# Performance work log

Hardware: AMD Instinct MI355X
Metric: run time of the kernel (lower is better)

Reference implementation:

```python
import jax, jax.numpy as jnp
import numpy as np
from jax import lax

B, C, L, H = 32, 256, 1280, 5
D = L // H  # head dim = 256
EPS = 1e-5


def setup_inputs() -> dict:
    key = jax.random.key(0)
    ks = jax.random.split(key, 16)
    s = 0.02
    inp = {
        "x": jax.random.normal(ks[0], (B, C, L), jnp.float32),
        # rank encoder Linear(L, L)
        "re_w": jax.random.normal(ks[1], (L, L), jnp.float32) * s,
        "re_b": jnp.zeros((L,), jnp.float32),
        # layer norms
        "ln1_g": jnp.ones((L,), jnp.float32), "ln1_b": jnp.zeros((L,), jnp.float32),
        "ln2_g": jnp.ones((L,), jnp.float32), "ln2_b": jnp.zeros((L,), jnp.float32),
        # attention projections (stored [in, out]; y @ W + b)
        "wq": jax.random.normal(ks[2], (L, L), jnp.float32) * s, "bq": jnp.zeros((L,), jnp.float32),
        "wk": jax.random.normal(ks[3], (L, L), jnp.float32) * s, "bk": jnp.zeros((L,), jnp.float32),
        "wv": jax.random.normal(ks[4], (L, L), jnp.float32) * s, "bv": jnp.zeros((L,), jnp.float32),
        "wo": jax.random.normal(ks[5], (L, L), jnp.float32) * s, "bo": jnp.zeros((L,), jnp.float32),
        # FFN (ffn_size == hidden_size == L in this module)
        "ffn_w1": jax.random.normal(ks[6], (L, L), jnp.float32) * s, "ffn_b1": jnp.zeros((L,), jnp.float32),
        "ffn_w2": jax.random.normal(ks[7], (L, L), jnp.float32) * s, "ffn_b2": jnp.zeros((L,), jnp.float32),
        # Conv1d(C, C, k=3, stride=1, pad=1, bias=False) + BatchNorm1d (eval) + ReLU
        "conv_w": jax.random.normal(ks[8], (C, C, 3), jnp.float32) * (2.0 / (C * 3)) ** 0.5,
        "bn_g": jnp.ones((C,), jnp.float32), "bn_b": jnp.zeros((C,), jnp.float32),
        "bn_m": jnp.zeros((C,), jnp.float32), "bn_v": jnp.ones((C,), jnp.float32),
    }
    return inp


def _layernorm(t, g, b):
    m = jnp.mean(t, axis=-1, keepdims=True)
    v = jnp.var(t, axis=-1, keepdims=True)
    return (t - m) * lax.rsqrt(v + EPS) * g + b


def reference(x, re_w, re_b, ln1_g, ln1_b, ln2_g, ln2_b,
              wq, bq, wk, bk, wv, bv, wo, bo,
              ffn_w1, ffn_b1, ffn_w2, ffn_b2,
              conv_w, bn_g, bn_b, bn_m, bn_v):
    b_, c_, l_ = x.shape
    # _getrank_: rank from double argsort (descending), mapped to (L - rank)/L
    rank_i = jnp.argsort(jnp.argsort(-x, axis=-1), axis=-1)
    rank = (l_ - rank_i).astype(x.dtype) / l_
    node = x + rank @ re_w + re_b                      # [B, C, L]

    # EncoderLayer: pre-LN MHSA (attn_bias is None in this call path)
    y = _layernorm(node, ln1_g, ln1_b)
    scale = D ** -0.5
    q = (y @ wq + bq).reshape(b_, c_, H, D).transpose(0, 2, 1, 3) * scale  # [B,H,C,D]
    k = (y @ wk + bk).reshape(b_, c_, H, D).transpose(0, 2, 1, 3)
    v = (y @ wv + bv).reshape(b_, c_, H, D).transpose(0, 2, 1, 3)
    attn = jax.nn.softmax(jnp.einsum('bhqd,bhkd->bhqk', q, k), axis=-1)   # [B,H,C,C]
    o = jnp.einsum('bhqk,bhkd->bhqd', attn, v)
    o = o.transpose(0, 2, 1, 3).reshape(b_, c_, l_) @ wo + bo
    h = node + o  # dropout is identity in eval

    # FFN sublayer
    y2 = _layernorm(h, ln2_g, ln2_b)
    f = jax.nn.gelu(y2 @ ffn_w1 + ffn_b1, approximate=False) @ ffn_w2 + ffn_b2
    h = h + f                                           # [B, C, L]

    # ConvBNRelu: Conv1d(k=3, s=1, p=1, no bias) -> BN (eval stats) -> ReLU
    conv = lax.conv_general_dilated(h, conv_w, window_strides=(1,),
                                    padding=[(1, 1)],
                                    dimension_numbers=('NCH', 'OIH', 'NCH'))
    bn = (conv - bn_m[None, :, None]) * lax.rsqrt(bn_v[None, :, None] + EPS)
    bn = bn * bn_g[None, :, None] + bn_b[None, :, None]
    return jax.nn.relu(bn)
```

## Files before the change

### kernel.cpp

```cpp
#include <hip/hip_runtime.h>
#include <hip/hip_bf16.h>
#include <stdint.h>

#define L_   1280
#define B_   32
#define C_   256
#define H_   5
#define D_   256
#define BC_  8192
#define EPSV 1e-5f

typedef __attribute__((ext_vector_type(8))) short bf16x8;
typedef __attribute__((ext_vector_type(4))) float f32x4;
typedef __hip_bfloat16 bf16;

__device__ __forceinline__ bf16 f2bf(float v) { return __float2bfloat16(v); }

#define GLDS16(gptr, lptr)                                                        \
    __builtin_amdgcn_global_load_lds(                                             \
        (const __attribute__((address_space(1))) void*)(gptr),                    \
        (__attribute__((address_space(3))) void*)(lptr), 16, 0, 0)

struct WtArgs { const float* src[7]; bf16* dst[7]; };

__global__ __launch_bounds__(256) void transpose7(WtArgs a) {
    const int mat = blockIdx.z;
    const float* src = a.src[mat];
    bf16* dst = a.dst[mat];
    __shared__ float tile[32][33];
    const int bx = blockIdx.x * 32;
    const int by = blockIdx.y * 32;
    const int tx = threadIdx.x, ty = threadIdx.y;
    #pragma unroll
    for (int r = ty; r < 32; r += 8)
        tile[r][tx] = src[(size_t)(by + r) * L_ + bx + tx];
    __syncthreads();
    #pragma unroll
    for (int r = ty; r < 32; r += 8)
        dst[(size_t)(bx + r) * L_ + by + tx] = f2bf(tile[tx][r]);
}

__global__ __launch_bounds__(256) void prep_conv(const float* cw, const float* g, const float* b,
                                                 const float* m, const float* v,
                                                 bf16* WT, float* sc, float* bi) {
    const int i = blockIdx.x * 256 + threadIdx.x;
    if (i < 3 * 256 * 256) {
        const int co = i / 768;
        const int r = i - co * 768;
        const int t = r >> 8, ci = r & 255;
        WT[i] = f2bf(cw[(co * 256 + ci) * 3 + t]);
    }
    if (i < 256) {
        const float s = g[i] * rsqrtf(v[i] + EPSV);
        sc[i] = s;
        bi[i] = b[i] - m[i] * s;
    }
}

__global__ __launch_bounds__(256) void rank_kernel(const float* __restrict__ x, bf16* __restrict__ R) {
    __shared__ float vals[L_];
    __shared__ float sv[L_];
    __shared__ int hist[256];
    __shared__ int pfx[256];
    __shared__ int cur[256];
    const int row = blockIdx.x, tid = threadIdx.x;
    const float* src = x + (size_t)row * L_;
    for (int i = tid; i < L_; i += 256) vals[i] = src[i];
    hist[tid] = 0;
    __syncthreads();
    float myv[5]; int myb[5];
    #pragma unroll
    for (int ii = 0; ii < 5; ii++) {
        const float v = vals[tid + ii * 256];
        int bk = (int)((4.0f - v) * 32.0f);
        bk = bk < 0 ? 0 : (bk > 255 ? 255 : bk);
        myv[ii] = v; myb[ii] = bk;
        atomicAdd(&hist[bk], 1);
    }
    __syncthreads();
    pfx[tid] = hist[tid];
    __syncthreads();
    for (int off = 1; off < 256; off <<= 1) {
        int t = (tid >= off) ? pfx[tid - off] : 0;
        __syncthreads();
        pfx[tid] += t;
        __syncthreads();
    }
    cur[tid] = pfx[tid] - hist[tid];
    __syncthreads();
    #pragma unroll
    for (int ii = 0; ii < 5; ii++) {
        const int pos = atomicAdd(&cur[myb[ii]], 1);
        sv[pos] = myv[ii];
    }
    __syncthreads();
    #pragma unroll
    for (int ii = 0; ii < 5; ii++) {
        const int bk = myb[ii]; const float v = myv[ii];
        const int s = pfx[bk] - hist[bk], e = pfx[bk];
        int cg = s;
        for (int p = s; p < e; p++) cg += (sv[p] > v) ? 1 : 0;
        R[(size_t)row * L_ + tid + ii * 256] = f2bf((float)(L_ - cg) * (1.0f / L_));
    }
}

__global__ __launch_bounds__(256) void ln_kernel(const float* __restrict__ in,
                                                 const float* __restrict__ g,
                                                 const float* __restrict__ b,
                                                 bf16* __restrict__ out) {
    const int row = blockIdx.x, tid = threadIdx.x;
    const float* src = in + (size_t)row * L_;
    float4 va = ((const float4*)src)[tid];
    float s = va.x + va.y + va.z + va.w;
    float ss = va.x * va.x + va.y * va.y + va.z * va.z + va.w * va.w;
    float4 vb = {0, 0, 0, 0};
    if (tid < 64) {
        vb = ((const float4*)src)[256 + tid];
        s += vb.x + vb.y + vb.z + vb.w;
        ss += vb.x * vb.x + vb.y * vb.y + vb.z * vb.z + vb.w * vb.w;
    }
    #pragma unroll
    for (int off = 32; off > 0; off >>= 1) {
        s += __shfl_down(s, off, 64);
        ss += __shfl_down(ss, off, 64);
    }
    __shared__ float rs[4], rss[4];
    __shared__ float mean_s, rstd_s;
    if ((tid & 63) == 0) { rs[tid >> 6] = s; rss[tid >> 6] = ss; }
    __syncthreads();
    if (tid == 0) {
        const float S = rs[0] + rs[1] + rs[2] + rs[3];
        const float SS = rss[0] + rss[1] + rss[2] + rss[3];
        const float m = S * (1.0f / L_);
        const float var = SS * (1.0f / L_) - m * m;
        mean_s = m; rstd_s = rsqrtf(var + EPSV);
    }
    __syncthreads();
    const float m = mean_s, r = rstd_s;
    {
        const int c = tid * 4;
        bf16 t4[4];
        t4[0] = f2bf((va.x - m) * r * g[c + 0] + b[c + 0]);
        t4[1] = f2bf((va.y - m) * r * g[c + 1] + b[c + 1]);
        t4[2] = f2bf((va.z - m) * r * g[c + 2] + b[c + 2]);
        t4[3] = f2bf((va.w - m) * r * g[c + 3] + b[c + 3]);
        *(uint2*)(out + (size_t)row * L_ + c) = *(uint2*)t4;
    }
    if (tid < 64) {
        const int c = 1024 + tid * 4;
        bf16 t4[4];
        t4[0] = f2bf((vb.x - m) * r * g[c + 0] + b[c + 0]);
        t4[1] = f2bf((vb.y - m) * r * g[c + 1] + b[c + 1]);
        t4[2] = f2bf((vb.z - m) * r * g[c + 2] + b[c + 2]);
        t4[3] = f2bf((vb.w - m) * r * g[c + 3] + b[c + 3]);
        *(uint2*)(out + (size_t)row * L_ + c) = *(uint2*)t4;
    }
}

__global__ __launch_bounds__(256) void softmax_kernel(const bf16* __restrict__ S, bf16* __restrict__ P) {
    const int row = blockIdx.x * 4 + (threadIdx.x >> 6);
    const int l = threadIdx.x & 63;
    const bf16* src = S + (size_t)row * 256 + l * 4;
    uint2 raw = *(const uint2*)src;
    bf16 s4[4]; *(uint2*)s4 = raw;
    float v0 = __bfloat162float(s4[0]), v1 = __bfloat162float(s4[1]);
    float v2 = __bfloat162float(s4[2]), v3 = __bfloat162float(s4[3]);
    float mx = fmaxf(fmaxf(v0, v1), fmaxf(v2, v3));
    #pragma unroll
    for (int off = 1; off < 64; off <<= 1) mx = fmaxf(mx, __shfl_xor(mx, off, 64));
    const float e0 = expf(v0 - mx), e1 = expf(v1 - mx), e2 = expf(v2 - mx), e3 = expf(v3 - mx);
    float sm = e0 + e1 + e2 + e3;
    #pragma unroll
    for (int off = 1; off < 64; off <<= 1) sm += __shfl_xor(sm, off, 64);
    const float inv = 1.0f / sm;
    bf16 t4[4] = { f2bf(e0 * inv), f2bf(e1 * inv), f2bf(e2 * inv), f2bf(e3 * inv) };
    *(uint2*)(P + (size_t)row * 256 + l * 4) = *(uint2*)t4;
}

__global__ __launch_bounds__(256) void zero_pads(bf16* h2T) {
    const int i = blockIdx.x * 256 + threadIdx.x;
    const int b = i >> 9;
    const int which = (i >> 8) & 1;
    const int ci = i & 255;
    const long row = which ? 1281 : 0;
    h2T[(long)b * (1282 * 256) + row * 256 + ci] = f2bf(0.0f);
}

struct GemmP {
    const bf16* A;  long lda, sA1, sA2;
    const bf16* Bt; long ldb, sB1, sB2;
    int zmod;
    int K;
    float* outF; bf16* outB; bf16* outB2; bf16* outB3; long ldc, sC1, sC2;
    const float* bias; const float* bias2; const float* bias3;
    const float* res; long ldres, sR1, sR2;
    const float* rowscale; const float* rowbias;
    float scale;
};

constexpr int E_F32_BIAS_RES = 0;
constexpr int E_F32 = 4;
constexpr int E_BF16 = 5;
constexpr int E_GELU = 6;
constexpr int E_FFN2T = 7;
constexpr int E_CONVBNR = 8;
constexpr int E_QKV = 9;

template <int EPI>
__global__ __launch_bounds__(256) void gemm_bt(GemmP p) {
    const int nwg  = gridDim.x * gridDim.y * gridDim.z;
    const int orig = (blockIdx.z * gridDim.y + blockIdx.y) * gridDim.x + blockIdx.x;
    int bx, rowg;
    if ((nwg & 7) == 0) {
        const int chunk = nwg >> 3;
        const int xcd = orig & 7, pos = orig >> 3;
        const int rpc = chunk / gridDim.x;
        if (rpc * gridDim.x == chunk) {
            bx   = pos / rpc;
            rowg = xcd * rpc + (pos - bx * rpc);
        } else {
            const int wgid = xcd * chunk + pos;
            bx = wgid % gridDim.x; rowg = wgid / gridDim.x;
        }
    } else {
        bx = blockIdx.x; rowg = blockIdx.z * gridDim.y + blockIdx.y;
    }
    const int by = rowg % gridDim.y;
    const int bz = rowg / gridDim.y;

    const int zq = bz / p.zmod, zr = bz % p.zmod;
    const bf16* A  = p.A  + (long)zq * p.sA1 + (long)zr * p.sA2;
    const bf16* Bt = p.Bt + (long)zq * p.sB1 + (long)zr * p.sB2;
    const int row0 = by * 128, col0 = bx * 128;

    __shared__ __align__(16) bf16 shm[16384];

    const int tid = threadIdx.x;
    const int l = tid & 63, w = tid >> 6;
    const int wr = w >> 1, wc = w & 1;

    f32x4 acc[4][4];
    #pragma unroll
    for (int m = 0; m < 4; m++)
        #pragma unroll
        for (int n = 0; n < 4; n++)
            acc[m][n] = (f32x4){0.f, 0.f, 0.f, 0.f};

    const bf16* gA = A  + (long)(row0 + w * 16 + (l >> 2)) * p.lda + (l & 3) * 8;
    const bf16* gB = Bt + (long)(col0 + w * 16 + (l >> 2)) * p.ldb + (l & 3) * 8;
    const long aStep = 64 * p.lda, bStep = 64 * p.ldb;

    auto STAGE = [&](int buf) {
        bf16* lA = shm + buf * 4096;
        bf16* lB = shm + 8192 + buf * 4096;
        GLDS16(gA,         lA + w * 512);
        GLDS16(gA + aStep, lA + 2048 + w * 512);
        GLDS16(gB,         lB + w * 512);
        GLDS16(gB + bStep, lB + 2048 + w * 512);
        gA += 32; gB += 32;
    };
    auto COMPUTE = [&](int buf) {
        const bf16* lA = shm + buf * 4096;
        const bf16* lB = shm + 8192 + buf * 4096;
        bf16x8 aF[4], bF[4];
        #pragma unroll
        for (int m = 0; m < 4; m++)
            aF[m] = *(const bf16x8*)(lA + (wr * 64 + m * 16 + (l & 15)) * 32 + (l >> 4) * 8);
        #pragma unroll
        for (int n = 0; n < 4; n++)
            bF[n] = *(const bf16x8*)(lB + (wc * 64 + n * 16 + (l & 15)) * 32 + (l >> 4) * 8);
        #pragma unroll
        for (int m = 0; m < 4; m++)
            #pragma unroll
            for (int n = 0; n < 4; n++)
                acc[m][n] = __builtin_amdgcn_mfma_f32_16x16x32_bf16(aF[m], bF[n], acc[m][n], 0, 0, 0);
    };

    const int nt = p.K >> 5;
    STAGE(0);
    int cur = 0;
    for (int t = 0; t < nt - 1; ++t) {
        STAGE(cur ^ 1);
        asm volatile("s_waitcnt vmcnt(4)" ::: "memory");
        __builtin_amdgcn_sched_barrier(0);
        __builtin_amdgcn_s_barrier();
        COMPUTE(cur);
        __builtin_amdgcn_sched_barrier(0);
        __builtin_amdgcn_s_barrier();
        cur ^= 1;
    }
    asm volatile("s_waitcnt vmcnt(0)" ::: "memory");
    __builtin_amdgcn_sched_barrier(0);
    __builtin_amdgcn_s_barrier();
    COMPUTE(cur);

    if constexpr (EPI == E_QKV) {
        if (col0 >= 2560) {
            const int v0  = col0 - 2560;
            const int hh  = v0 >> 8;
            const int dd0 = v0 & 255;
            const int b_  = row0 >> 8;
            const int c0b = row0 & 255;
            __syncthreads();
            #pragma unroll
            for (int m = 0; m < 4; m++)
                #pragma unroll
                for (int n = 0; n < 4; n++) {
                    const int cc = wc * 64 + n * 16 + (l & 15);
                    const float bb = p.bias3[v0 + cc];
                    #pragma unroll
                    for (int j = 0; j < 4; j++) {
                        const int r = wr * 64 + m * 16 + (l >> 4) * 4 + j;
                        shm[cc * 128 + (r ^ ((cc & 7) << 3))] = f2bf(acc[m][n][j] + bb);
                    }
                }
            __syncthreads();
            const int d = tid >> 1, ch = (tid & 1) * 64;
            bf16* dstRow = p.outB3 +
                (((long)((b_ * H_ + hh) * 256 + dd0 + d)) << 8) + c0b;
            #pragma unroll
            for (int g = 0; g < 8; g++) {
                const int rb = ch + g * 8;
                *(bf16x8*)(dstRow + rb) =
                    *(const bf16x8*)&shm[d * 128 + (rb ^ ((d & 7) << 3))];
            }
            return;
        }
    }

    const long cz = (long)zq * p.sC1 + (long)zr * p.sC2;
    const long rz = (long)zq * p.sR1 + (long)zr * p.sR2;
    #pragma unroll
    for (int m = 0; m < 4; m++) {
        #pragma unroll
        for (int n = 0; n < 4; n++) {
            const int gcol = col0 + wc * 64 + n * 16 + (l & 15);
            #pragma unroll
            for (int j = 0; j < 4; j++) {
                const int grow = row0 + wr * 64 + m * 16 + (l >> 4) * 4 + j;
                const float v = acc[m][n][j];
                if constexpr (EPI == E_F32_BIAS_RES) {
                    p.outF[cz + (long)grow * p.ldc + gcol] =
                        v + p.bias[gcol] + p.res[rz + (long)grow * p.ldres + gcol];
                } else if constexpr (EPI == E_F32) {
                    p.outF[cz + (long)grow * p.ldc + gcol] = v;
                } else if constexpr (EPI == E_BF16) {
                    p.outB[cz + (long)grow * p.ldc + gcol] = f2bf(v);
                } else if constexpr (EPI == E_GELU) {
                    const float t = v + p.bias[gcol];
                    p.outB[cz + (long)grow * p.ldc + gcol] =
                        f2bf(0.5f * t * (1.0f + erff(t * 0.70710678f)));
                } else if constexpr (EPI == E_FFN2T) {
                    const float t = v + p.bias[gcol] + p.res[rz + (long)grow * p.ldres + gcol];
                    const int b_ = grow >> 8, ci = grow & 255;
                    p.outB[(long)b_ * (1282 * 256) + (long)(gcol + 1) * 256 + ci] = f2bf(t);
                } else if constexpr (EPI == E_CONVBNR) {
                    const float t = v * p.rowscale[grow] + p.rowbias[grow];
                    p.outF[cz + (long)grow * p.ldc + gcol] = fmaxf(t, 0.0f);
                } else if constexpr (EPI == E_QKV) {
                    if (gcol < 1280) {
                        p.outB[(long)grow * L_ + gcol] = f2bf((v + p.bias[gcol]) * p.scale);
                    } else {
                        const int c2 = gcol - 1280;
                        p.outB2[(long)grow * L_ + c2] = f2bf(v + p.bias2[c2]);
                    }
                }
            }
        }
    }
}

extern "C" void kernel_launch(void* const* d_in, const int* in_sizes, int n_in,
                              void* d_out, int out_size, void* d_ws, size_t ws_size,
                              hipStream_t stream) {
    const float* x    = (const float*)d_in[0];
    const float* re_w = (const float*)d_in[1];
    const float* re_b = (const float*)d_in[2];
    const float* ln1g = (const float*)d_in[3];
    const float* ln1b = (const float*)d_in[4];
    const float* ln2g = (const float*)d_in[5];
    const float* ln2b = (const float*)d_in[6];
    const float* wq   = (const float*)d_in[7];
    const float* bq   = (const float*)d_in[8];
    const float* wk   = (const float*)d_in[9];
    const float* bk   = (const float*)d_in[10];
    const float* wv   = (const float*)d_in[11];
    const float* bv   = (const float*)d_in[12];
    const float* wo   = (const float*)d_in[13];
    const float* bo   = (const float*)d_in[14];
    const float* fw1  = (const float*)d_in[15];
    const float* fb1  = (const float*)d_in[16];
    const float* fw2  = (const float*)d_in[17];
    const float* fb2  = (const float*)d_in[18];
    const float* convw = (const float*)d_in[19];
    const float* bng  = (const float*)d_in[20];
    const float* bnb  = (const float*)d_in[21];
    const float* bnm  = (const float*)d_in[22];
    const float* bnv  = (const float*)d_in[23];
    float* out = (float*)d_out;

    char* ws = (char*)d_ws;
    const size_t SZ_WT     = (size_t)L_ * L_ * 2;
    const size_t SZ_ACT_BF = (size_t)BC_ * L_ * 2;
    const size_t SZ_ACT_F  = (size_t)BC_ * L_ * 4;
    const size_t SZ_H2T    = (size_t)B_ * 1282 * 256 * 2;
    const size_t SZ_S      = (size_t)160 * 256 * 256 * 4;

    size_t off = 0;
    bf16* Wt[7];
    for (int i = 0; i < 7; i++) { Wt[i] = (bf16*)(ws + off); off += SZ_WT; }
    bf16* WconvT   = (bf16*)(ws + off); off += 393216;
    float* bnscale = (float*)(ws + off); off += 1024;
    float* bnbias  = (float*)(ws + off); off += 1024;
    bf16* RP  = (bf16*)(ws + off); off += SZ_ACT_BF;
    bf16* Yb  = (bf16*)(ws + off); off += SZ_ACT_BF;
    bf16* Qb  = (bf16*)(ws + off); off += SZ_ACT_BF;
    bf16* Kb  = (bf16*)(ws + off); off += SZ_H2T;
    float* Sb = (float*)(ws + off); off += SZ_S;
    float* node = (float*)(ws + off); off += SZ_ACT_F;
    bf16* Sbf = (bf16*)Sb;
    bf16* VT  = Sbf + (size_t)160 * 65536;
    (void)in_sizes; (void)n_in; (void)out_size;

    if (ws_size < off) return;

    WtArgs wa;
    wa.src[0] = re_w; wa.src[1] = wq; wa.src[2] = wk; wa.src[3] = wv;
    wa.src[4] = wo;  wa.src[5] = fw1; wa.src[6] = fw2;
    for (int i = 0; i < 7; i++) wa.dst[i] = Wt[i];
    transpose7<<<dim3(40, 40, 7), dim3(32, 8), 0, stream>>>(wa);
    prep_conv<<<dim3(768), 256, 0, stream>>>(convw, bng, bnb, bnm, bnv, WconvT, bnscale, bnbias);

    rank_kernel<<<dim3(BC_), 256, 0, stream>>>(x, RP);

    const dim3 gBig(L_ / 128, BC_ / 128, 1);
    const dim3 gQKV(3840 / 128, BC_ / 128, 1);
    const dim3 gAttn(2, 2, 160);
    const dim3 blk(256);

    {
        GemmP p{}; p.zmod = 1; p.K = L_;
        p.A = RP; p.lda = L_; p.Bt = Wt[0]; p.ldb = L_;
        p.outF = node; p.ldc = L_; p.bias = re_b; p.res = x; p.ldres = L_;
        gemm_bt<E_F32_BIAS_RES><<<gBig, blk, 0, stream>>>(p);
    }
    ln_kernel<<<dim3(BC_), blk, 0, stream>>>(node, ln1g, ln1b, Yb);
    {
        GemmP p{}; p.zmod = 1; p.K = L_;
        p.A = Yb; p.lda = L_; p.Bt = Wt[1]; p.ldb = L_;
        p.outB = Qb; p.outB2 = Kb; p.outB3 = VT;
        p.bias = bq; p.bias2 = bk; p.bias3 = bv; p.scale = 0.0625f;
        gemm_bt<E_QKV><<<gQKV, blk, 0, stream>>>(p);
    }
    {
        GemmP p{}; p.zmod = H_; p.K = 256;
        p.A = Qb;  p.lda = L_; p.sA1 = (long)C_ * L_; p.sA2 = 256;
        p.Bt = Kb; p.ldb = L_; p.sB1 = (long)C_ * L_; p.sB2 = 256;
        p.outB = Sbf; p.ldc = 256; p.sC1 = (long)H_ * 65536; p.sC2 = 65536;
        gemm_bt<E_BF16><<<gAttn, blk, 0, stream>>>(p);
    }
    softmax_kernel<<<dim3(160 * 256 / 4), blk, 0, stream>>>(Sbf, RP);
    {
        GemmP p{}; p.zmod = H_; p.K = 256;
        p.A = RP;  p.lda = 256; p.sA1 = (long)H_ * 65536; p.sA2 = 65536;
        p.Bt = VT; p.ldb = 256; p.sB1 = (long)H_ * 65536; p.sB2 = 65536;
        p.outB = Qb; p.ldc = L_; p.sC1 = (long)C_ * L_; p.sC2 = 256;
        gemm_bt<E_BF16><<<gAttn, blk, 0, stream>>>(p);
    }
    {
        GemmP p{}; p.zmod = 1; p.K = L_;
        p.A = Qb; p.lda = L_; p.Bt = Wt[4]; p.ldb = L_;
        p.outF = node; p.ldc = L_; p.bias = bo; p.res = node; p.ldres = L_;
        gemm_bt<E_F32_BIAS_RES><<<gBig, blk, 0, stream>>>(p);
    }
    ln_kernel<<<dim3(BC_), blk, 0, stream>>>(node, ln2g, ln2b, RP);
    {
        GemmP p{}; p.zmod = 1; p.K = L_;
        p.A = RP; p.lda = L_; p.Bt = Wt[5]; p.ldb = L_;
        p.outB = Yb; p.ldc = L_; p.bias = fb1;
        gemm_bt<E_GELU><<<gBig, blk, 0, stream>>>(p);
    }
    zero_pads<<<dim3(64), blk, 0, stream>>>(Kb);
    {
        GemmP p{}; p.zmod = 1; p.K = L_;
        p.A = Yb; p.lda = L_; p.Bt = Wt[6]; p.ldb = L_;
        p.outB = Kb; p.bias = fb2; p.res = node; p.ldres = L_;
        gemm_bt<E_FFN2T><<<gBig, blk, 0, stream>>>(p);
    }
    {
        GemmP p{}; p.zmod = 1; p.K = 768;
        p.A = WconvT; p.lda = 768;
        p.Bt = Kb; p.ldb = 256; p.sB1 = 1282 * 256;
        p.outF = out; p.ldc = L_; p.sC1 = (long)C_ * L_;
        p.rowscale = bnscale; p.rowbias = bnbias;
        gemm_bt<E_CONVBNR><<<dim3(L_ / 128, 2, B_), blk, 0, stream>>>(p);
    }
}
```

Before: 541.9 us.

## Triple-buffer GEMM LDS staging and store residual stream in bf16

The GEMM main loop moves from double to triple buffering in LDS. Loads are issued two tiles ahead and one barrier per iteration is dropped, so global-to-LDS latency overlaps better with MFMA compute. Separately, the residual activation 'node' is now stored and read as bf16 instead of fp32, halving traffic in the residual epilogues and the layernorm kernels. This costs precision in the residual path and raises LDS use per block, which may lower occupancy.

```diff
diff --git a/kernel.cpp b/kernel.cpp
--- a/kernel.cpp
+++ b/kernel.cpp
@@ -15,6 +15,7 @@
 typedef __hip_bfloat16 bf16;
 
 __device__ __forceinline__ bf16 f2bf(float v) { return __float2bfloat16(v); }
+__device__ __forceinline__ float bf2f(bf16 v) { return __bfloat162float(v); }
 
 #define GLDS16(gptr, lptr)                                                        \
     __builtin_amdgcn_global_load_lds(                                             \
@@ -104,20 +105,24 @@
     }
 }
 
-__global__ __launch_bounds__(256) void ln_kernel(const float* __restrict__ in,
+__global__ __launch_bounds__(256) void ln_kernel(const bf16* __restrict__ in,
                                                  const float* __restrict__ g,
                                                  const float* __restrict__ b,
                                                  bf16* __restrict__ out) {
     const int row = blockIdx.x, tid = threadIdx.x;
-    const float* src = in + (size_t)row * L_;
-    float4 va = ((const float4*)src)[tid];
-    float s = va.x + va.y + va.z + va.w;
-    float ss = va.x * va.x + va.y * va.y + va.z * va.z + va.w * va.w;
-    float4 vb = {0, 0, 0, 0};
+    const bf16* src = in + (size_t)row * L_;
+    uint2 ra = ((const uint2*)src)[tid];
+    bf16 a4[4]; *(uint2*)a4 = ra;
+    const float a0 = bf2f(a4[0]), a1 = bf2f(a4[1]), a2 = bf2f(a4[2]), a3 = bf2f(a4[3]);
+    float s = a0 + a1 + a2 + a3;
+    float ss = a0 * a0 + a1 * a1 + a2 * a2 + a3 * a3;
+    float b0 = 0, b1 = 0, b2 = 0, b3 = 0;
     if (tid < 64) {
-        vb = ((const float4*)src)[256 + tid];
-        s += vb.x + vb.y + vb.z + vb.w;
-        ss += vb.x * vb.x + vb.y * vb.y + vb.z * vb.z + vb.w * vb.w;
+        uint2 rb = ((const uint2*)src)[256 + tid];
+        bf16 b4[4]; *(uint2*)b4 = rb;
+        b0 = bf2f(b4[0]); b1 = bf2f(b4[1]); b2 = bf2f(b4[2]); b3 = bf2f(b4[3]);
+        s += b0 + b1 + b2 + b3;
+        ss += b0 * b0 + b1 * b1 + b2 * b2 + b3 * b3;
     }
     #pragma unroll
     for (int off = 32; off > 0; off >>= 1) {
@@ -140,19 +145,19 @@
     {
         const int c = tid * 4;
         bf16 t4[4];
-        t4[0] = f2bf((va.x - m) * r * g[c + 0] + b[c + 0]);
-        t4[1] = f2bf((va.y - m) * r * g[c + 1] + b[c + 1]);
-        t4[2] = f2bf((va.z - m) * r * g[c + 2] + b[c + 2]);
-        t4[3] = f2bf((va.w - m) * r * g[c + 3] + b[c + 3]);
+        t4[0] = f2bf((a0 - m) * r * g[c + 0] + b[c + 0]);
+        t4[1] = f2bf((a1 - m) * r * g[c + 1] + b[c + 1]);
+        t4[2] = f2bf((a2 - m) * r * g[c + 2] + b[c + 2]);
+        t4[3] = f2bf((a3 - m) * r * g[c + 3] + b[c + 3]);
         *(uint2*)(out + (size_t)row * L_ + c) = *(uint2*)t4;
     }
     if (tid < 64) {
         const int c = 1024 + tid * 4;
         bf16 t4[4];
-        t4[0] = f2bf((vb.x - m) * r * g[c + 0] + b[c + 0]);
-        t4[1] = f2bf((vb.y - m) * r * g[c + 1] + b[c + 1]);
-        t4[2] = f2bf((vb.z - m) * r * g[c + 2] + b[c + 2]);
-        t4[3] = f2bf((vb.w - m) * r * g[c + 3] + b[c + 3]);
+        t4[0] = f2bf((b0 - m) * r * g[c + 0] + b[c + 0]);
+        t4[1] = f2bf((b1 - m) * r * g[c + 1] + b[c + 1]);
+        t4[2] = f2bf((b2 - m) * r * g[c + 2] + b[c + 2]);
+        t4[3] = f2bf((b3 - m) * r * g[c + 3] + b[c + 3]);
         *(uint2*)(out + (size_t)row * L_ + c) = *(uint2*)t4;
     }
 }
@@ -163,8 +168,8 @@
     const bf16* src = S + (size_t)row * 256 + l * 4;
     uint2 raw = *(const uint2*)src;
     bf16 s4[4]; *(uint2*)s4 = raw;
-    float v0 = __bfloat162float(s4[0]), v1 = __bfloat162float(s4[1]);
-    float v2 = __bfloat162float(s4[2]), v3 = __bfloat162float(s4[3]);
+    float v0 = bf2f(s4[0]), v1 = bf2f(s4[1]);
+    float v2 = bf2f(s4[2]), v3 = bf2f(s4[3]);
     float mx = fmaxf(fmaxf(v0, v1), fmaxf(v2, v3));
     #pragma unroll
     for (int off = 1; off < 64; off <<= 1) mx = fmaxf(mx, __shfl_xor(mx, off, 64));
@@ -193,13 +198,13 @@
     int K;
     float* outF; bf16* outB; bf16* outB2; bf16* outB3; long ldc, sC1, sC2;
     const float* bias; const float* bias2; const float* bias3;
-    const float* res; long ldres, sR1, sR2;
+    const float* res; const bf16* resB; long ldres, sR1, sR2;
     const float* rowscale; const float* rowbias;
     float scale;
 };
 
-constexpr int E_F32_BIAS_RES = 0;
-constexpr int E_F32 = 4;
+constexpr int E_NODE = 0;
+constexpr int E_HRES = 1;
 constexpr int E_BF16 = 5;
 constexpr int E_GELU = 6;
 constexpr int E_FFN2T = 7;
@@ -233,7 +238,7 @@
     const bf16* Bt = p.Bt + (long)zq * p.sB1 + (long)zr * p.sB2;
     const int row0 = by * 128, col0 = bx * 128;
 
-    __shared__ __align__(16) bf16 shm[16384];
+    __shared__ __align__(16) bf16 shm[24576];
 
     const int tid = threadIdx.x;
     const int l = tid & 63, w = tid >> 6;
@@ -252,7 +257,7 @@
 
     auto STAGE = [&](int buf) {
         bf16* lA = shm + buf * 4096;
-        bf16* lB = shm + 8192 + buf * 4096;
+        bf16* lB = shm + 12288 + buf * 4096;
         GLDS16(gA,         lA + w * 512);
         GLDS16(gA + aStep, lA + 2048 + w * 512);
         GLDS16(gB,         lB + w * 512);
@@ -261,7 +266,7 @@
     };
     auto COMPUTE = [&](int buf) {
         const bf16* lA = shm + buf * 4096;
-        const bf16* lB = shm + 8192 + buf * 4096;
+        const bf16* lB = shm + 12288 + buf * 4096;
         bf16x8 aF[4], bF[4];
         #pragma unroll
         for (int m = 0; m < 4; m++)
@@ -277,22 +282,21 @@
     };
 
     const int nt = p.K >> 5;
-    STAGE(0);
-    int cur = 0;
+    STAGE(0); STAGE(1);
+    int cb = 0, sb = 2;
     for (int t = 0; t < nt - 1; ++t) {
-        STAGE(cur ^ 1);
         asm volatile("s_waitcnt vmcnt(4)" ::: "memory");
         __builtin_amdgcn_sched_barrier(0);
         __builtin_amdgcn_s_barrier();
-        COMPUTE(cur);
-        __builtin_amdgcn_sched_barrier(0);
-        __builtin_amdgcn_s_barrier();
-        cur ^= 1;
+        if (t + 2 < nt) STAGE(sb);
+        COMPUTE(cb);
+        cb = (cb == 2) ? 0 : cb + 1;
+        sb = (sb == 2) ? 0 : sb + 1;
     }
     asm volatile("s_waitcnt vmcnt(0)" ::: "memory");
     __builtin_amdgcn_sched_barrier(0);
     __builtin_amdgcn_s_barrier();
-    COMPUTE(cur);
+    COMPUTE(cb);
 
     if constexpr (EPI == E_QKV) {
         if (col0 >= 2560) {
@@ -339,11 +343,12 @@
             for (int j = 0; j < 4; j++) {
                 const int grow = row0 + wr * 64 + m * 16 + (l >> 4) * 4 + j;
                 const float v = acc[m][n][j];
-                if constexpr (EPI == E_F32_BIAS_RES) {
-                    p.outF[cz + (long)grow * p.ldc + gcol] =
-                        v + p.bias[gcol] + p.res[rz + (long)grow * p.ldres + gcol];
-                } else if constexpr (EPI == E_F32) {
-                    p.outF[cz + (long)grow * p.ldc + gcol] = v;
+                if constexpr (EPI == E_NODE) {
+                    p.outB[cz + (long)grow * p.ldc + gcol] =
+                        f2bf(v + p.bias[gcol] + p.res[rz + (long)grow * p.ldres + gcol]);
+                } else if constexpr (EPI == E_HRES) {
+                    p.outB[cz + (long)grow * p.ldc + gcol] =
+                        f2bf(v + p.bias[gcol] + bf2f(p.resB[rz + (long)grow * p.ldres + gcol]));
                 } else if constexpr (EPI == E_BF16) {
                     p.outB[cz + (long)grow * p.ldc + gcol] = f2bf(v);
                 } else if constexpr (EPI == E_GELU) {
@@ -351,7 +356,8 @@
                     p.outB[cz + (long)grow * p.ldc + gcol] =
                         f2bf(0.5f * t * (1.0f + erff(t * 0.70710678f)));
                 } else if constexpr (EPI == E_FFN2T) {
-                    const float t = v + p.bias[gcol] + p.res[rz + (long)grow * p.ldres + gcol];
+                    const float t = v + p.bias[gcol] +
+                                    bf2f(p.resB[rz + (long)grow * p.ldres + gcol]);
                     const int b_ = grow >> 8, ci = grow & 255;
                     p.outB[(long)b_ * (1282 * 256) + (long)(gcol + 1) * 256 + ci] = f2bf(t);
                 } else if constexpr (EPI == E_CONVBNR) {
@@ -402,7 +408,6 @@
     char* ws = (char*)d_ws;
     const size_t SZ_WT     = (size_t)L_ * L_ * 2;
     const size_t SZ_ACT_BF = (size_t)BC_ * L_ * 2;
-    const size_t SZ_ACT_F  = (size_t)BC_ * L_ * 4;
     const size_t SZ_H2T    = (size_t)B_ * 1282 * 256 * 2;
     const size_t SZ_S      = (size_t)160 * 256 * 256 * 4;
 
@@ -417,7 +422,7 @@
     bf16* Qb  = (bf16*)(ws + off); off += SZ_ACT_BF;
     bf16* Kb  = (bf16*)(ws + off); off += SZ_H2T;
     float* Sb = (float*)(ws + off); off += SZ_S;
-    float* node = (float*)(ws + off); off += SZ_ACT_F;
+    bf16* nodeB = (bf16*)(ws + off); off += SZ_ACT_BF;
     bf16* Sbf = (bf16*)Sb;
     bf16* VT  = Sbf + (size_t)160 * 65536;
     (void)in_sizes; (void)n_in; (void)out_size;
@@ -441,10 +446,10 @@
     {
         GemmP p{}; p.zmod = 1; p.K = L_;
         p.A = RP; p.lda = L_; p.Bt = Wt[0]; p.ldb = L_;
-        p.outF = node; p.ldc = L_; p.bias = re_b; p.res = x; p.ldres = L_;
-        gemm_bt<E_F32_BIAS_RES><<<gBig, blk, 0, stream>>>(p);
-    }
-    ln_kernel<<<dim3(BC_), blk, 0, stream>>>(node, ln1g, ln1b, Yb);
+        p.outB = nodeB; p.ldc = L_; p.bias = re_b; p.res = x; p.ldres = L_;
+        gemm_bt<E_NODE><<<gBig, blk, 0, stream>>>(p);
+    }
+    ln_kernel<<<dim3(BC_), blk, 0, stream>>>(nodeB, ln1g, ln1b, Yb);
     {
         GemmP p{}; p.zmod = 1; p.K = L_;
         p.A = Yb; p.lda = L_; p.Bt = Wt[1]; p.ldb = L_;
@@ -470,10 +475,10 @@
     {
         GemmP p{}; p.zmod = 1; p.K = L_;
         p.A = Qb; p.lda = L_; p.Bt = Wt[4]; p.ldb = L_;
-        p.outF = node; p.ldc = L_; p.bias = bo; p.res = node; p.ldres = L_;
-        gemm_bt<E_F32_BIAS_RES><<<gBig, blk, 0, stream>>>(p);
-    }
-    ln_kernel<<<dim3(BC_), blk, 0, stream>>>(node, ln2g, ln2b, RP);
+        p.outB = nodeB; p.ldc = L_; p.bias = bo; p.resB = nodeB; p.ldres = L_;
+        gemm_bt<E_HRES><<<gBig, blk, 0, stream>>>(p);
+    }
+    ln_kernel<<<dim3(BC_), blk, 0, stream>>>(nodeB, ln2g, ln2b, RP);
     {
         GemmP p{}; p.zmod = 1; p.K = L_;
         p.A = RP; p.lda = L_; p.Bt = Wt[5]; p.ldb = L_;
@@ -484,7 +489,7 @@
     {
         GemmP p{}; p.zmod = 1; p.K = L_;
         p.A = Yb; p.lda = L_; p.Bt = Wt[6]; p.ldb = L_;
-        p.outB = Kb; p.bias = fb2; p.res = node; p.ldres = L_;
+        p.outB = Kb; p.bias = fb2; p.resB = nodeB; p.ldres = L_;
         gemm_bt<E_FFN2T><<<gBig, blk, 0, stream>>>(p);
     }
     {
```

New measurement: 520.4 us. 1.04x faster.
